# Kernel tuning notes

Measured on AMD Instinct MI355X. Metric: run time of the kernel, lower is better.

## Reference

```python
import jax, jax.numpy as jnp
import numpy as np

HEADS = 16
SCALE = 8.0
EPS = 1e-12  # F.normalize eps for fp32


def _l2norm(t):
    # F.normalize(t, dim=-1): t / max(||t||, eps)
    n = jnp.sqrt(jnp.sum(t * t, axis=-1, keepdims=True))
    return t / jnp.maximum(n, EPS)


def setup_inputs() -> dict:
    key = jax.random.key(0)
    k0, k1, k2, k3, k4 = jax.random.split(key, 5)
    b, n, d = 1, 4096, 1024
    w_scale = 1.0 / np.sqrt(d)
    return {
        "x": jax.random.normal(k0, (b, n, d), dtype=jnp.float32),
        "Wq": jax.random.normal(k1, (d, d), dtype=jnp.float32) * w_scale,
        "Wk": jax.random.normal(k2, (d, d), dtype=jnp.float32) * w_scale,
        "Wv": jax.random.normal(k3, (d, d), dtype=jnp.float32) * w_scale,
        "Wo": jax.random.normal(k4, (d, d), dtype=jnp.float32) * w_scale,
    }


def reference(x, Wq, Wk, Wv, Wo):
    b, n, d = x.shape
    h = HEADS
    dh = d // h
    # projections (nn.Linear without bias): y = x @ W  (W stored as [in, out])
    def proj(W):
        y = jnp.einsum('bnd,df->bnf', x, W)
        return y.reshape(b, n, h, dh).transpose(0, 2, 1, 3)  # b h n dh
    q, k, v = proj(Wq), proj(Wk), proj(Wv)
    # cosine-sim attention: L2-normalize q, k along head dim
    q = _l2norm(q)
    k = _l2norm(k)
    sim = jnp.einsum('bhid,bhjd->bhij', q, k) * SCALE
    mask_value = -jnp.finfo(sim.dtype).max
    causal = jnp.triu(jnp.ones((n, n), dtype=bool), 1)
    sim = jnp.where(causal, mask_value, sim)
    attn = jax.nn.softmax(sim, axis=-1)
    o = jnp.einsum('bhij,bhjd->bhid', attn, v)
    o = o.transpose(0, 2, 1, 3).reshape(b, n, d)  # b n (h dh)
    return jnp.einsum('bnf,fd->bnd', o, Wo)
```

## Files before the change

kernel.cpp:

```cpp
#include <hip/hip_runtime.h>
#include <stdint.h>
#include <math.h>

typedef __bf16 bf16_t;
typedef __attribute__((ext_vector_type(8))) __bf16 bf16x8;
typedef __attribute__((ext_vector_type(4))) __bf16 bf16x4;
typedef __attribute__((ext_vector_type(4))) float f32x4;

#define N_TOK 4096
#define D_MODEL 1024
#define HEADS 16
#define DH 64
#define C1 11.541560327111707f
#define C2 11.721897207207671f

__device__ __forceinline__ void async_copy16(const void* g, void* l) {
    __builtin_amdgcn_global_load_lds(
        (const __attribute__((address_space(1))) unsigned int*)g,
        (__attribute__((address_space(3))) unsigned int*)l, 16, 0, 0);
}

__global__ __launch_bounds__(256) void cast_x_kernel(const float* __restrict__ x,
                                                     bf16_t* __restrict__ xb) {
    int i = (blockIdx.x * 256 + threadIdx.x) * 4;
    float4 v = *(const float4*)(x + i);
    bf16x4 o;
    o[0] = (bf16_t)v.x; o[1] = (bf16_t)v.y; o[2] = (bf16_t)v.z; o[3] = (bf16_t)v.w;
    *(bf16x4*)(xb + i) = o;
}

__global__ __launch_bounds__(256) void transpose_w_kernel(
    const float* __restrict__ W0, const float* __restrict__ W1,
    const float* __restrict__ W2, const float* __restrict__ W3,
    bf16_t* __restrict__ T0, bf16_t* __restrict__ T1,
    bf16_t* __restrict__ T2, bf16_t* __restrict__ T3) {
    __shared__ bf16_t t[64][72];
    const float* W; bf16_t* T;
    switch (blockIdx.z) {
        case 0: W = W0; T = T0; break;
        case 1: W = W1; T = T1; break;
        case 2: W = W2; T = T2; break;
        default: W = W3; T = T3; break;
    }
    int k0 = blockIdx.x * 64, n0 = blockIdx.y * 64;
    int tx = threadIdx.x & 63, ty = threadIdx.x >> 6;
#pragma unroll
    for (int i = 0; i < 16; i++) {
        int kl = ty * 16 + i;
        t[kl][tx] = (bf16_t)W[(size_t)(k0 + kl) * D_MODEL + n0 + tx];
    }
    __syncthreads();
#pragma unroll
    for (int i = 0; i < 16; i++) {
        int nl = ty * 16 + i;
        T[(size_t)(n0 + nl) * D_MODEL + k0 + tx] = t[tx][nl];
    }
}

template <int WRITE_F32, int NORM>
__global__ __launch_bounds__(256) void gemm_tile(const bf16_t* __restrict__ A,
                                                 const bf16_t* __restrict__ Bt,
                                                 void* __restrict__ Cout, int ldc) {
    constexpr int K = D_MODEL;
    __shared__ __align__(16) bf16_t As[128 * 32];
    __shared__ __align__(16) bf16_t Bs[128 * 32];
    const int tid = threadIdx.x;
    const int m0 = blockIdx.y * 128;
    const int n0 = blockIdx.x * 128;
    const int wave = tid >> 6;
    const int lane = tid & 63;
    const int l15 = lane & 15;
    const int quad = lane >> 4;
    const int wm = (wave >> 1) * 64;
    const int wn = (wave & 1) * 64;
    f32x4 acc[4][4] = {};

    const int srow = tid >> 2;
    const int soff = (tid & 3) * 8;
    const bf16_t* gA = A + (size_t)(m0 + srow) * K + soff;
    const bf16_t* gB = Bt + (size_t)(n0 + srow) * K + soff;
    bf16_t* lA = &As[tid * 8];
    bf16_t* lB = &Bs[tid * 8];
    constexpr int HGAP = 64 * K;

    for (int kt = 0; kt < K; kt += 32) {
        __syncthreads();
        async_copy16(gA + kt, lA);
        async_copy16(gA + HGAP + kt, lA + 2048);
        async_copy16(gB + kt, lB);
        async_copy16(gB + HGAP + kt, lB + 2048);
        __syncthreads();
        bf16x8 af[4], bfr[4];
#pragma unroll
        for (int mi = 0; mi < 4; mi++)
            af[mi] = *(const bf16x8*)(&As[(wm + mi * 16 + l15) * 32 + quad * 8]);
#pragma unroll
        for (int ni = 0; ni < 4; ni++)
            bfr[ni] = *(const bf16x8*)(&Bs[(wn + ni * 16 + l15) * 32 + quad * 8]);
#pragma unroll
        for (int mi = 0; mi < 4; mi++)
#pragma unroll
            for (int ni = 0; ni < 4; ni++)
                acc[mi][ni] = __builtin_amdgcn_mfma_f32_16x16x32_bf16(
                    af[mi], bfr[ni], acc[mi][ni], 0, 0, 0);
    }

    if (NORM && n0 < 2048) {
#pragma unroll
        for (int mi = 0; mi < 4; mi++)
#pragma unroll
            for (int r = 0; r < 4; r++) {
                float s = 0.f;
#pragma unroll
                for (int ni = 0; ni < 4; ni++) {
                    float v = acc[mi][ni][r];
                    s += v * v;
                }
                s += __shfl_xor(s, 1);
                s += __shfl_xor(s, 2);
                s += __shfl_xor(s, 4);
                s += __shfl_xor(s, 8);
                float sc = 1.0f / fmaxf(sqrtf(s), 1e-12f);
#pragma unroll
                for (int ni = 0; ni < 4; ni++) acc[mi][ni][r] *= sc;
            }
    }
#pragma unroll
    for (int mi = 0; mi < 4; mi++)
#pragma unroll
        for (int ni = 0; ni < 4; ni++)
#pragma unroll
            for (int r = 0; r < 4; r++) {
                int row = m0 + wm + mi * 16 + quad * 4 + r;
                int col = n0 + wn + ni * 16 + l15;
                float v = acc[mi][ni][r];
                if (WRITE_F32)
                    ((float*)Cout)[(size_t)row * ldc + col] = v;
                else
                    ((bf16_t*)Cout)[(size_t)row * ldc + col] = (bf16_t)v;
            }
}

__global__ __launch_bounds__(256) void transpose_v_kernel(const bf16_t* __restrict__ QKV,
                                                          bf16_t* __restrict__ Vt) {
    __shared__ bf16_t t[64][72];
    int n0 = blockIdx.x * 64;
    int h = blockIdx.y;
    int tx = threadIdx.x & 63, ty = threadIdx.x >> 6;
#pragma unroll
    for (int i = 0; i < 16; i++) {
        int nl = ty * 16 + i;
        t[nl][tx] = QKV[(size_t)(n0 + nl) * 3072 + 2048 + h * DH + tx];
    }
    __syncthreads();
    const int e = tx & 7, q = (tx >> 3) & 3;
    const int J = (tx & 32) + 16 * (e >> 2) + 4 * q + (e & 3);
#pragma unroll
    for (int i = 0; i < 16; i++) {
        int dl = ty * 16 + i;
        Vt[(size_t)(h * DH + dl) * N_TOK + n0 + tx] = t[J][dl];
    }
}

__global__ __launch_bounds__(256) void attn_kernel(const bf16_t* __restrict__ QKV,
                                                   const bf16_t* __restrict__ Vt,
                                                   bf16_t* __restrict__ O) {
    __shared__ __align__(16) bf16_t Ks[2][4096];
    __shared__ __align__(16) bf16_t Vs[2][2][2048];
    const int tid = threadIdx.x;
    const int wave = tid >> 6;
    const int lane = tid & 63;
    const int l15 = lane & 15;
    const int quad = lane >> 4;

    const int xcd = blockIdx.x & 7;
    const int hb = (blockIdx.x >> 3) & 1;
    const int jj = (blockIdx.x >> 4) & 15;
    const int ph2 = blockIdx.x >> 8;
    const int h = xcd * 2 + hb;
    const int u = ph2 ? 31 - jj : jj;
    const int g1 = 63 - u;
    const int g0 = u;

    const bool heavy = wave < 2;
    const int wg = wave & 1;
    const int g_my = heavy ? g1 : g0;
    const int ib0 = wg * 2;
    const int i_base = g_my * 64 + wg * 32;

    const bf16_t* Qb = QKV + h * DH;
    const bf16_t* Kb = QKV + 1024 + h * DH;
    const bf16_t* Vb = Vt + (size_t)h * DH * N_TOK;

    bf16x8 aq[2][2];
#pragma unroll
    for (int s = 0; s < 2; s++)
#pragma unroll
        for (int kd = 0; kd < 2; kd++)
            aq[s][kd] = *(const bf16x8*)(Qb + (size_t)(i_base + s * 16 + l15) * 3072 +
                                         kd * 32 + quad * 8);

    f32x4 od[2][4] = {};
    float l_acc[2] = {0.f, 0.f};

    const int krow = tid >> 3;
    const int kc = (tid & 7) ^ (krow & 7);
    const bf16_t* gK = Kb + (size_t)krow * 3072 + kc * 8;
    const int vd = tid >> 2;
    const int vc = (tid & 3) ^ ((vd >> 1) & 3);
    const bf16_t* gV = Vb + (size_t)vd * N_TOK + vc * 8;

    async_copy16(gK, &Ks[0][tid * 8]);
    async_copy16(gK + (size_t)32 * 3072, &Ks[0][tid * 8 + 2048]);
    async_copy16(gV, &Vs[0][0][tid * 8]);
    async_copy16(gV + 32, &Vs[0][1][tid * 8]);

    const int ksw = l15 & 7;
    const int vsw = (l15 >> 1) & 3;

    for (int jt = 0; jt <= g1; jt++) {
        __syncthreads();
        if (jt < g1) {
            const int b = (jt + 1) & 1;
            const bf16_t* kn = gK + (size_t)(jt + 1) * 64 * 3072;
            async_copy16(kn, &Ks[b][tid * 8]);
            async_copy16(kn + (size_t)32 * 3072, &Ks[b][tid * 8 + 2048]);
            async_copy16(gV + (jt + 1) * 64, &Vs[b][0][tid * 8]);
            async_copy16(gV + (jt + 1) * 64 + 32, &Vs[b][1][tid * 8]);
        }
        if (!heavy && jt > g0) continue;
        const bf16_t* KS = Ks[jt & 1];
        const bool diag = (jt == g_my);
        const int jm0 = diag ? ib0 : 3;
        const int jm1 = diag ? ib0 + 1 : 3;

        bf16x8 ak[4][2];
#pragma unroll
        for (int jh = 0; jh < 4; jh++) {
            if (jh > jm1) continue;
#pragma unroll
            for (int kd = 0; kd < 2; kd++)
                ak[jh][kd] = *(const bf16x8*)(&KS[(jh * 16 + l15) * 64 +
                                                  (((kd * 4 + quad) ^ ksw) * 8)]);
        }
        f32x4 sj[2][4] = {};
#pragma unroll
        for (int kd = 0; kd < 2; kd++)
#pragma unroll
            for (int jh = 0; jh < 4; jh++)
#pragma unroll
                for (int s = 0; s < 2; s++) {
                    if (jh > (diag ? ib0 + s : 3)) continue;
                    sj[s][jh] = __builtin_amdgcn_mfma_f32_16x16x32_bf16(
                        ak[jh][kd], aq[s][kd], sj[s][jh], 0, 0, 0);
                }

        float p[2][4][4] = {};
#pragma unroll
        for (int s = 0; s < 2; s++) {
#pragma unroll
            for (int jh = 0; jh < 4; jh++) {
                if (jh > (diag ? ib0 + s : 3)) continue;
                if (diag && jh == ib0 + s) {
#pragma unroll
                    for (int r = 0; r < 4; r++) {
                        float v = (quad * 4 + r > l15) ? 0.f
                                  : __builtin_amdgcn_exp2f(sj[s][jh][r] * C1 - C2);
                        p[s][jh][r] = v;
                        l_acc[s] += v;
                    }
                } else {
#pragma unroll
                    for (int r = 0; r < 4; r++) {
                        float v = __builtin_amdgcn_exp2f(sj[s][jh][r] * C1 - C2);
                        p[s][jh][r] = v;
                        l_acc[s] += v;
                    }
                }
            }
        }
        bf16x8 pk8[2][2];
#pragma unroll
        for (int s = 0; s < 2; s++)
#pragma unroll
            for (int H = 0; H < 2; H++)
#pragma unroll
                for (int r = 0; r < 4; r++) {
                    pk8[s][H][r] = (bf16_t)p[s][2 * H][r];
                    pk8[s][H][4 + r] = (bf16_t)p[s][2 * H + 1][r];
                }

        const bf16_t* VS0 = Vs[jt & 1][0];
#pragma unroll
        for (int mt = 0; mt < 4; mt++) {
            bf16x8 vf = *(const bf16x8*)(&VS0[(mt * 16 + l15) * 32 + ((quad ^ vsw) * 8)]);
            od[0][mt] = __builtin_amdgcn_mfma_f32_16x16x32_bf16(vf, pk8[0][0], od[0][mt], 0, 0, 0);
            od[1][mt] = __builtin_amdgcn_mfma_f32_16x16x32_bf16(vf, pk8[1][0], od[1][mt], 0, 0, 0);
        }
        if (jm1 >= 2) {
            const bf16_t* VS1 = Vs[jt & 1][1];
#pragma unroll
            for (int mt = 0; mt < 4; mt++) {
                bf16x8 vf = *(const bf16x8*)(&VS1[(mt * 16 + l15) * 32 + ((quad ^ vsw) * 8)]);
                if (jm0 >= 2)
                    od[0][mt] = __builtin_amdgcn_mfma_f32_16x16x32_bf16(vf, pk8[0][1], od[0][mt], 0, 0, 0);
                od[1][mt] = __builtin_amdgcn_mfma_f32_16x16x32_bf16(vf, pk8[1][1], od[1][mt], 0, 0, 0);
            }
        }
    }

#pragma unroll
    for (int s = 0; s < 2; s++) {
        float l = l_acc[s];
        l += __shfl_xor(l, 16);
        l += __shfl_xor(l, 32);
        float inv = 1.0f / l;
#pragma unroll
        for (int mt = 0; mt < 4; mt++) {
            bf16x4 o;
#pragma unroll
            for (int r = 0; r < 4; r++) o[r] = (bf16_t)(od[s][mt][r] * inv);
            *(bf16x4*)(&O[(size_t)(i_base + s * 16 + l15) * D_MODEL + h * DH +
                          mt * 16 + quad * 4]) = o;
        }
    }
}

extern "C" void kernel_launch(void* const* d_in, const int* in_sizes, int n_in,
                              void* d_out, int out_size, void* d_ws, size_t ws_size,
                              hipStream_t stream) {
    const float* x  = (const float*)d_in[0];
    const float* Wq = (const float*)d_in[1];
    const float* Wk = (const float*)d_in[2];
    const float* Wv = (const float*)d_in[3];
    const float* Wo = (const float*)d_in[4];
    float* out = (float*)d_out;
    char* ws = (char*)d_ws;
    const size_t MB = 1024 * 1024;
    bf16_t* xb   = (bf16_t*)(ws);
    bf16_t* Wt3  = (bf16_t*)(ws + 8 * MB);
    bf16_t* Wot  = (bf16_t*)(ws + 14 * MB);
    bf16_t* QKV  = (bf16_t*)(ws + 16 * MB);
    bf16_t* Vt   = (bf16_t*)(ws + 40 * MB);
    bf16_t* Ob   = (bf16_t*)(ws + 48 * MB);

    cast_x_kernel<<<4096, 256, 0, stream>>>(x, xb);
    dim3 gw(16, 16, 4);
    transpose_w_kernel<<<gw, 256, 0, stream>>>(Wq, Wk, Wv, Wo,
                                               Wt3, Wt3 + 1024 * 1024, Wt3 + 2 * 1024 * 1024, Wot);
    dim3 gqkv(3072 / 128, N_TOK / 128);
    gemm_tile<0, 1><<<gqkv, 256, 0, stream>>>(xb, Wt3, QKV, 3072);
    dim3 gv(N_TOK / 64, HEADS);
    transpose_v_kernel<<<gv, 256, 0, stream>>>(QKV, Vt);
    attn_kernel<<<512, 256, 0, stream>>>(QKV, Vt, Ob);
    dim3 go(D_MODEL / 128, N_TOK / 128);
    gemm_tile<1, 0><<<go, 256, 0, stream>>>(Ob, Wot, out, D_MODEL);
}
```

Before: 246.5 us.

## Split KV tiles across wave pairs with pipelined QK/PV and MFMA row sums

The attention block no longer splits its waves into a heavy pair and a light pair. Instead each block walks both query tiles (63-u, then u) in turn, and the two wave pairs alternate KV tiles by parity. A triple-buffered LDS ring lets the P·V step for the previous tile overlap with QK^T for the current one. Partial outputs and row sums are combined through LDS at the end. Row sums now come from an MFMA against a ones vector, and the softmax scale is folded into the Q normalization in the projection GEMM, dropping the constant offset and a multiply-add per exp. This balances work across waves, but it adds an LDS reduction, extra barriers and a larger LDS footprint, and removing the offset relies on bounded cosine logits to avoid overflow.

```diff
diff --git a/kernel.cpp b/kernel.cpp
--- a/kernel.cpp
+++ b/kernel.cpp
@@ -12,7 +12,6 @@
 #define HEADS 16
 #define DH 64
 #define C1 11.541560327111707f
-#define C2 11.721897207207671f
 
 __device__ __forceinline__ void async_copy16(const void* g, void* l) {
     __builtin_amdgcn_global_load_lds(
@@ -106,6 +105,7 @@
     }
 
     if (NORM && n0 < 2048) {
+        const float post = (n0 < 1024) ? C1 : 1.0f;
 #pragma unroll
         for (int mi = 0; mi < 4; mi++)
 #pragma unroll
@@ -120,7 +120,7 @@
                 s += __shfl_xor(s, 2);
                 s += __shfl_xor(s, 4);
                 s += __shfl_xor(s, 8);
-                float sc = 1.0f / fmaxf(sqrtf(s), 1e-12f);
+                float sc = post / fmaxf(sqrtf(s), 1e-12f);
 #pragma unroll
                 for (int ni = 0; ni < 4; ni++) acc[mi][ni][r] *= sc;
             }
@@ -165,43 +165,25 @@
 __global__ __launch_bounds__(256) void attn_kernel(const bf16_t* __restrict__ QKV,
                                                    const bf16_t* __restrict__ Vt,
                                                    bf16_t* __restrict__ O) {
-    __shared__ __align__(16) bf16_t Ks[2][4096];
-    __shared__ __align__(16) bf16_t Vs[2][2][2048];
+    __shared__ __align__(16) bf16_t Ks[3][4096];
+    __shared__ __align__(16) bf16_t Vs[3][2][2048];
     const int tid = threadIdx.x;
     const int wave = tid >> 6;
     const int lane = tid & 63;
     const int l15 = lane & 15;
     const int quad = lane >> 4;
+    const int rh = wave & 1;
+    const int pw = wave >> 1;
+    const int ib0 = rh * 2;
 
     const int xcd = blockIdx.x & 7;
-    const int hb = (blockIdx.x >> 3) & 1;
-    const int jj = (blockIdx.x >> 4) & 15;
-    const int ph2 = blockIdx.x >> 8;
-    const int h = xcd * 2 + hb;
-    const int u = ph2 ? 31 - jj : jj;
-    const int g1 = 63 - u;
-    const int g0 = u;
-
-    const bool heavy = wave < 2;
-    const int wg = wave & 1;
-    const int g_my = heavy ? g1 : g0;
-    const int ib0 = wg * 2;
-    const int i_base = g_my * 64 + wg * 32;
+    const int t = blockIdx.x >> 3;
+    const int h = xcd * 2 + (t & 1);
+    const int u = t >> 1;
 
     const bf16_t* Qb = QKV + h * DH;
     const bf16_t* Kb = QKV + 1024 + h * DH;
     const bf16_t* Vb = Vt + (size_t)h * DH * N_TOK;
-
-    bf16x8 aq[2][2];
-#pragma unroll
-    for (int s = 0; s < 2; s++)
-#pragma unroll
-        for (int kd = 0; kd < 2; kd++)
-            aq[s][kd] = *(const bf16x8*)(Qb + (size_t)(i_base + s * 16 + l15) * 3072 +
-                                         kd * 32 + quad * 8);
-
-    f32x4 od[2][4] = {};
-    float l_acc[2] = {0.f, 0.f};
 
     const int krow = tid >> 3;
     const int kc = (tid & 7) ^ (krow & 7);
@@ -210,119 +192,164 @@
     const int vc = (tid & 3) ^ ((vd >> 1) & 3);
     const bf16_t* gV = Vb + (size_t)vd * N_TOK + vc * 8;
 
-    async_copy16(gK, &Ks[0][tid * 8]);
-    async_copy16(gK + (size_t)32 * 3072, &Ks[0][tid * 8 + 2048]);
-    async_copy16(gV, &Vs[0][0][tid * 8]);
-    async_copy16(gV + 32, &Vs[0][1][tid * 8]);
-
     const int ksw = l15 & 7;
     const int vsw = (l15 >> 1) & 3;
 
-    for (int jt = 0; jt <= g1; jt++) {
-        __syncthreads();
-        if (jt < g1) {
-            const int b = (jt + 1) & 1;
-            const bf16_t* kn = gK + (size_t)(jt + 1) * 64 * 3072;
-            async_copy16(kn, &Ks[b][tid * 8]);
-            async_copy16(kn + (size_t)32 * 3072, &Ks[b][tid * 8 + 2048]);
-            async_copy16(gV + (jt + 1) * 64, &Vs[b][0][tid * 8]);
-            async_copy16(gV + (jt + 1) * 64 + 32, &Vs[b][1][tid * 8]);
+    bf16x8 vone;
+#pragma unroll
+    for (int i = 0; i < 8; i++) vone[i] = (bf16_t)1.0f;
+
+    for (int ph = 0; ph < 2; ph++) {
+        const int g = ph ? u : 63 - u;
+        const int i_base = g * 64 + rh * 32;
+
+        bf16x8 aq[2][2];
+#pragma unroll
+        for (int s = 0; s < 2; s++)
+#pragma unroll
+            for (int kd = 0; kd < 2; kd++)
+                aq[s][kd] = *(const bf16x8*)(Qb + (size_t)(i_base + s * 16 + l15) * 3072 +
+                                             kd * 32 + quad * 8);
+
+        f32x4 od[2][4] = {};
+        f32x4 lv[2] = {};
+        bf16x8 pk8[2][2];
+
+        async_copy16(gK, &Ks[0][tid * 8]);
+        async_copy16(gK + (size_t)32 * 3072, &Ks[0][tid * 8 + 2048]);
+        async_copy16(gV, &Vs[0][0][tid * 8]);
+        async_copy16(gV + 32, &Vs[0][1][tid * 8]);
+
+        int cur = 0, nxt = 1, prv = 2;
+        for (int it = 0; it <= g + 1; ++it) {
+            __syncthreads();
+            if (it < g) {
+                const bf16_t* kn = gK + (size_t)(it + 1) * 64 * 3072;
+                async_copy16(kn, &Ks[nxt][tid * 8]);
+                async_copy16(kn + (size_t)32 * 3072, &Ks[nxt][tid * 8 + 2048]);
+                async_copy16(gV + (it + 1) * 64, &Vs[nxt][0][tid * 8]);
+                async_copy16(gV + (it + 1) * 64 + 32, &Vs[nxt][1][tid * 8]);
+            }
+
+            if (it >= 1 && ((it - 1) & 1) == pw) {
+                const bool diagB = ((it - 1) == g);
+                const bf16_t* VS0 = Vs[prv][0];
+#pragma unroll
+                for (int mt = 0; mt < 4; mt++) {
+                    bf16x8 vf = *(const bf16x8*)(&VS0[(mt * 16 + l15) * 32 + ((quad ^ vsw) * 8)]);
+                    od[0][mt] = __builtin_amdgcn_mfma_f32_16x16x32_bf16(vf, pk8[0][0], od[0][mt], 0, 0, 0);
+                    od[1][mt] = __builtin_amdgcn_mfma_f32_16x16x32_bf16(vf, pk8[1][0], od[1][mt], 0, 0, 0);
+                }
+                if (!(diagB && rh == 0)) {
+                    const bf16_t* VS1 = Vs[prv][1];
+#pragma unroll
+                    for (int mt = 0; mt < 4; mt++) {
+                        bf16x8 vf = *(const bf16x8*)(&VS1[(mt * 16 + l15) * 32 + ((quad ^ vsw) * 8)]);
+                        od[0][mt] = __builtin_amdgcn_mfma_f32_16x16x32_bf16(vf, pk8[0][1], od[0][mt], 0, 0, 0);
+                        od[1][mt] = __builtin_amdgcn_mfma_f32_16x16x32_bf16(vf, pk8[1][1], od[1][mt], 0, 0, 0);
+                    }
+                }
+            }
+
+            if (it <= g && (it & 1) == pw) {
+                const bool diagA = (it == g);
+                const bf16_t* KS = Ks[cur];
+                const int jmax = diagA ? ib0 + 1 : 3;
+                bf16x8 ak[4][2];
+#pragma unroll
+                for (int jh = 0; jh < 4; jh++) {
+                    if (jh > jmax) continue;
+#pragma unroll
+                    for (int kd = 0; kd < 2; kd++)
+                        ak[jh][kd] = *(const bf16x8*)(&KS[(jh * 16 + l15) * 64 +
+                                                          (((kd * 4 + quad) ^ ksw) * 8)]);
+                }
+                f32x4 sj[2][4] = {};
+#pragma unroll
+                for (int kd = 0; kd < 2; kd++)
+#pragma unroll
+                    for (int jh = 0; jh < 4; jh++)
+#pragma unroll
+                        for (int s = 0; s < 2; s++) {
+                            if (jh > (diagA ? ib0 + s : 3)) continue;
+                            sj[s][jh] = __builtin_amdgcn_mfma_f32_16x16x32_bf16(
+                                ak[jh][kd], aq[s][kd], sj[s][jh], 0, 0, 0);
+                        }
+
+                float p[2][4][4] = {};
+#pragma unroll
+                for (int s = 0; s < 2; s++) {
+#pragma unroll
+                    for (int jh = 0; jh < 4; jh++) {
+                        if (jh > (diagA ? ib0 + s : 3)) continue;
+                        if (diagA && jh == ib0 + s) {
+#pragma unroll
+                            for (int r = 0; r < 4; r++)
+                                p[s][jh][r] = (quad * 4 + r > l15) ? 0.f
+                                              : __builtin_amdgcn_exp2f(sj[s][jh][r]);
+                        } else {
+#pragma unroll
+                            for (int r = 0; r < 4; r++)
+                                p[s][jh][r] = __builtin_amdgcn_exp2f(sj[s][jh][r]);
+                        }
+                    }
+                }
+#pragma unroll
+                for (int s = 0; s < 2; s++)
+#pragma unroll
+                    for (int H = 0; H < 2; H++)
+#pragma unroll
+                        for (int r = 0; r < 4; r++) {
+                            pk8[s][H][r] = (bf16_t)p[s][2 * H][r];
+                            pk8[s][H][4 + r] = (bf16_t)p[s][2 * H + 1][r];
+                        }
+                lv[0] = __builtin_amdgcn_mfma_f32_16x16x32_bf16(vone, pk8[0][0], lv[0], 0, 0, 0);
+                lv[1] = __builtin_amdgcn_mfma_f32_16x16x32_bf16(vone, pk8[1][0], lv[1], 0, 0, 0);
+                if (!(diagA && rh == 0)) {
+                    lv[0] = __builtin_amdgcn_mfma_f32_16x16x32_bf16(vone, pk8[0][1], lv[0], 0, 0, 0);
+                    lv[1] = __builtin_amdgcn_mfma_f32_16x16x32_bf16(vone, pk8[1][1], lv[1], 0, 0, 0);
+                }
+            }
+
+            int tmp = prv; prv = cur; cur = nxt; nxt = tmp;
         }
-        if (!heavy && jt > g0) continue;
-        const bf16_t* KS = Ks[jt & 1];
-        const bool diag = (jt == g_my);
-        const int jm0 = diag ? ib0 : 3;
-        const int jm1 = diag ? ib0 + 1 : 3;
-
-        bf16x8 ak[4][2];
-#pragma unroll
-        for (int jh = 0; jh < 4; jh++) {
-            if (jh > jm1) continue;
-#pragma unroll
-            for (int kd = 0; kd < 2; kd++)
-                ak[jh][kd] = *(const bf16x8*)(&KS[(jh * 16 + l15) * 64 +
-                                                  (((kd * 4 + quad) ^ ksw) * 8)]);
+
+        __syncthreads();
+        float* red  = (float*)&Ks[0][0];
+        float* redl = (float*)&Vs[0][0][0];
+        if (pw == 1) {
+            const int base = rh * 2048;
+#pragma unroll
+            for (int s = 0; s < 2; s++)
+#pragma unroll
+                for (int mt = 0; mt < 4; mt++)
+                    *(f32x4*)&red[base + (s * 4 + mt) * 256 + lane * 4] = od[s][mt];
+            redl[rh * 128 + lane * 2 + 0] = lv[0][0];
+            redl[rh * 128 + lane * 2 + 1] = lv[1][0];
         }
-        f32x4 sj[2][4] = {};
-#pragma unroll
-        for (int kd = 0; kd < 2; kd++)
-#pragma unroll
-            for (int jh = 0; jh < 4; jh++)
-#pragma unroll
-                for (int s = 0; s < 2; s++) {
-                    if (jh > (diag ? ib0 + s : 3)) continue;
-                    sj[s][jh] = __builtin_amdgcn_mfma_f32_16x16x32_bf16(
-                        ak[jh][kd], aq[s][kd], sj[s][jh], 0, 0, 0);
-                }
-
-        float p[2][4][4] = {};
-#pragma unroll
-        for (int s = 0; s < 2; s++) {
-#pragma unroll
-            for (int jh = 0; jh < 4; jh++) {
-                if (jh > (diag ? ib0 + s : 3)) continue;
-                if (diag && jh == ib0 + s) {
-#pragma unroll
-                    for (int r = 0; r < 4; r++) {
-                        float v = (quad * 4 + r > l15) ? 0.f
-                                  : __builtin_amdgcn_exp2f(sj[s][jh][r] * C1 - C2);
-                        p[s][jh][r] = v;
-                        l_acc[s] += v;
-                    }
-                } else {
-#pragma unroll
-                    for (int r = 0; r < 4; r++) {
-                        float v = __builtin_amdgcn_exp2f(sj[s][jh][r] * C1 - C2);
-                        p[s][jh][r] = v;
-                        l_acc[s] += v;
-                    }
-                }
-            }
+        __syncthreads();
+        if (pw == 0) {
+            const int base = rh * 2048;
+#pragma unroll
+            for (int s = 0; s < 2; s++)
+#pragma unroll
+                for (int mt = 0; mt < 4; mt++)
+                    od[s][mt] += *(const f32x4*)&red[base + (s * 4 + mt) * 256 + lane * 4];
+            float linv[2];
+            linv[0] = 1.0f / (lv[0][0] + redl[rh * 128 + lane * 2 + 0]);
+            linv[1] = 1.0f / (lv[1][0] + redl[rh * 128 + lane * 2 + 1]);
+#pragma unroll
+            for (int s = 0; s < 2; s++)
+#pragma unroll
+                for (int mt = 0; mt < 4; mt++) {
+                    bf16x4 o;
+#pragma unroll
+                    for (int r = 0; r < 4; r++) o[r] = (bf16_t)(od[s][mt][r] * linv[s]);
+                    *(bf16x4*)(&O[(size_t)(i_base + s * 16 + l15) * D_MODEL + h * DH +
+                                  mt * 16 + quad * 4]) = o;
+                }
         }
-        bf16x8 pk8[2][2];
-#pragma unroll
-        for (int s = 0; s < 2; s++)
-#pragma unroll
-            for (int H = 0; H < 2; H++)
-#pragma unroll
-                for (int r = 0; r < 4; r++) {
-                    pk8[s][H][r] = (bf16_t)p[s][2 * H][r];
-                    pk8[s][H][4 + r] = (bf16_t)p[s][2 * H + 1][r];
-                }
-
-        const bf16_t* VS0 = Vs[jt & 1][0];
-#pragma unroll
-        for (int mt = 0; mt < 4; mt++) {
-            bf16x8 vf = *(const bf16x8*)(&VS0[(mt * 16 + l15) * 32 + ((quad ^ vsw) * 8)]);
-            od[0][mt] = __builtin_amdgcn_mfma_f32_16x16x32_bf16(vf, pk8[0][0], od[0][mt], 0, 0, 0);
-            od[1][mt] = __builtin_amdgcn_mfma_f32_16x16x32_bf16(vf, pk8[1][0], od[1][mt], 0, 0, 0);
-        }
-        if (jm1 >= 2) {
-            const bf16_t* VS1 = Vs[jt & 1][1];
-#pragma unroll
-            for (int mt = 0; mt < 4; mt++) {
-                bf16x8 vf = *(const bf16x8*)(&VS1[(mt * 16 + l15) * 32 + ((quad ^ vsw) * 8)]);
-                if (jm0 >= 2)
-                    od[0][mt] = __builtin_amdgcn_mfma_f32_16x16x32_bf16(vf, pk8[0][1], od[0][mt], 0, 0, 0);
-                od[1][mt] = __builtin_amdgcn_mfma_f32_16x16x32_bf16(vf, pk8[1][1], od[1][mt], 0, 0, 0);
-            }
-        }
-    }
-
-#pragma unroll
-    for (int s = 0; s < 2; s++) {
-        float l = l_acc[s];
-        l += __shfl_xor(l, 16);
-        l += __shfl_xor(l, 32);
-        float inv = 1.0f / l;
-#pragma unroll
-        for (int mt = 0; mt < 4; mt++) {
-            bf16x4 o;
-#pragma unroll
-            for (int r = 0; r < 4; r++) o[r] = (bf16_t)(od[s][mt][r] * inv);
-            *(bf16x4*)(&O[(size_t)(i_base + s * 16 + l15) * D_MODEL + h * DH +
-                          mt * 16 + quad * 4]) = o;
-        }
+        __syncthreads();
     }
 }
 
```

Measured after the change: 234.9 us. -4.7%, faster.
